# Kernel optimization log

Hardware: AMD Instinct MI355X
Metric: run time of the kernel (lower is better)

## Reference

```python
import jax, jax.numpy as jnp
import numpy as np
from jax import lax

DISP = 4   # max displacement for correlation -> 81 channels
KSZ = 3    # deform/gate conv kernel size


def conv2d(x, w, b=None):
    out = lax.conv_general_dilated(x, w, (1, 1), 'SAME',
                                   dimension_numbers=('NCHW', 'OIHW', 'NCHW'))
    if b is not None:
        out = out + b[None, :, None, None]
    return out


def correlation(x1, x2, d=DISP):
    # FlowNet-style cost volume, kernel_size=1: per-displacement channel-mean dot product.
    B, C, H, W = x1.shape
    x2p = jnp.pad(x2, ((0, 0), (0, 0), (d, d), (d, d)))
    outs = []
    for dy in range(2 * d + 1):
        for dx in range(2 * d + 1):
            shifted = lax.dynamic_slice(x2p, (0, 0, dy, dx), (B, C, H, W))
            outs.append(jnp.sum(x1 * shifted, axis=1) / C)
    return jnp.stack(outs, axis=1)  # [B, (2d+1)^2, H, W]


def bilinear_sample(img, y, x):
    # img: [B,C,H,W]; y,x: [B,H,W] float sample coords; zero padding outside.
    B, C, H, W = img.shape
    y0 = jnp.floor(y); x0 = jnp.floor(x)
    y1 = y0 + 1.0;     x1 = x0 + 1.0
    wy1 = y - y0; wx1 = x - x0
    wy0 = 1.0 - wy1; wx0 = 1.0 - wx1
    flat = img.reshape(B, C, H * W)

    def gather(yi, xi):
        valid = (yi >= 0) & (yi <= H - 1) & (xi >= 0) & (xi <= W - 1)
        yc = jnp.clip(yi, 0, H - 1).astype(jnp.int32)
        xc = jnp.clip(xi, 0, W - 1).astype(jnp.int32)
        idx = (yc * W + xc).reshape(B, 1, H * W)
        g = jnp.take_along_axis(flat, idx, axis=2).reshape(B, C, H, W)
        return g * valid.astype(img.dtype)[:, None]

    return (gather(y0, x0) * (wy0 * wx0)[:, None]
          + gather(y0, x1) * (wy0 * wx1)[:, None]
          + gather(y1, x0) * (wy1 * wx0)[:, None]
          + gather(y1, x1) * (wy1 * wx1)[:, None])


def deform_conv(img, offset, w, k=KSZ):
    # offset: [B, 2*k*k, H, W] with (dy, dx) pairs per kernel tap (row-major).
    B, C, H, W = img.shape
    pad = (k - 1) // 2
    ys = jnp.arange(H, dtype=img.dtype)[None, :, None]
    xs = jnp.arange(W, dtype=img.dtype)[None, None, :]
    out = jnp.zeros((B, w.shape[0], H, W), dtype=img.dtype)
    for kk in range(k * k):
        ky, kx = kk // k, kk % k
        y = ys + (ky - pad) + offset[:, 2 * kk]
        x = xs + (kx - pad) + offset[:, 2 * kk + 1]
        s = bilinear_sample(img, y, x)
        out = out + jnp.einsum('oc,bchw->bohw', w[:, :, ky, kx], s)
    return out


def linear_scale(x, std_multiplier=3.0):
    pos = x > 0
    cnt = jnp.sum(pos).astype(x.dtype)
    mean = jnp.sum(jnp.where(pos, x, 0.0)) / jnp.maximum(cnt, 1.0)
    var = jnp.sum(jnp.where(pos, (x - mean) ** 2, 0.0)) / jnp.maximum(cnt - 1.0, 1.0)
    ub = mean + std_multiplier * jnp.sqrt(var)
    ub = jnp.where(cnt >= 2.0, ub, 1.0)  # matches torch nan / empty-positive fallback
    return jnp.clip(x, 0.0, lax.stop_gradient(ub)) / ub


def setup_inputs() -> dict:
    key = jax.random.key(0)
    ks = jax.random.split(key, 10)
    B, C, H, W = 8, 256, 64, 64
    f = jnp.float32
    inp = {
        'inputs':   jax.random.normal(ks[0], (B, C, H, W), f),
        'in_state': jax.random.normal(ks[1], (B, C, H, W), f),
        'w_reset':  jax.random.normal(ks[2], (C, 2 * C, 3, 3), f) * 0.02,
        'b_reset':  jnp.zeros((C,), f),
        'w_update': jax.random.normal(ks[3], (C, 2 * C, 3, 3), f) * 0.02,
        'b_update': jnp.zeros((C,), f),
        'w_out':    jax.random.normal(ks[4], (C, 2 * C, 3, 3), f) * 0.02,
        'b_out':    jnp.zeros((C,), f),
        'w_offset': jax.random.normal(ks[5], (18, 81, 1, 1), f) * 0.01,
        'w_align':  jax.random.normal(ks[6], (C, C, 3, 3), f) * 0.01,
    }
    return inp


def reference(inputs, in_state, w_reset, b_reset, w_update, b_update,
              w_out, b_out, w_offset, w_align):
    # align_features: correlation -> 1x1 offset conv -> deformable conv
    corr = correlation(inputs, in_state)
    offset = conv2d(corr, w_offset)
    aligned = deform_conv(in_state, offset, w_align)
    # ConvGRU gates with linear-scaled relu gates
    stacked = jnp.concatenate([inputs, aligned], axis=1)
    update = linear_scale(jax.nn.relu(conv2d(stacked, w_update, b_update)))
    reset = linear_scale(jax.nn.relu(conv2d(stacked, w_reset, b_reset)))
    out_in = jax.nn.relu(conv2d(jnp.concatenate([inputs, in_state * reset], axis=1), w_out, b_out))
    new_state = in_state * (1.0 - update) + out_in * update
    return (new_state, new_state)  # (out_feat, new_state)
```

## Files before the change

kernel.cpp:

```cpp
#include <hip/hip_runtime.h>
#include <stdint.h>
#include <math.h>

typedef unsigned short u16;
typedef short bf16x8 __attribute__((ext_vector_type(8)));
typedef float f32x4 __attribute__((ext_vector_type(4)));

#define MFMA16x16x32(a,b,c) __builtin_amdgcn_mfma_f32_16x16x32_bf16((a),(b),(c),0,0,0)

typedef __attribute__((address_space(3))) void as3_void;
typedef const __attribute__((address_space(1))) void as1_void;

__device__ __forceinline__ void g2l16(const void* g, void* l){
#if __has_builtin(__builtin_amdgcn_global_load_lds)
  __builtin_amdgcn_global_load_lds((as1_void*)g, (as3_void*)l, 16, 0, 0);
#else
  *(int4*)l = *(const int4*)g;
#endif
}

__device__ __forceinline__ u16 f2bf(float f){
  uint32_t u = __builtin_bit_cast(uint32_t, f);
  u += 0x7fffu + ((u >> 16) & 1u);
  return (u16)(u >> 16);
}
__device__ __forceinline__ float bf2f(u16 h){
  uint32_t u = ((uint32_t)h) << 16;
  return __builtin_bit_cast(float, u);
}
__device__ __forceinline__ void unpack8(int4 v, float* o){
  uint32_t w0=(uint32_t)v.x, w1=(uint32_t)v.y, w2=(uint32_t)v.z, w3=(uint32_t)v.w;
  o[0]=__builtin_bit_cast(float, w0<<16); o[1]=__builtin_bit_cast(float, w0&0xffff0000u);
  o[2]=__builtin_bit_cast(float, w1<<16); o[3]=__builtin_bit_cast(float, w1&0xffff0000u);
  o[4]=__builtin_bit_cast(float, w2<<16); o[5]=__builtin_bit_cast(float, w2&0xffff0000u);
  o[6]=__builtin_bit_cast(float, w3<<16); o[7]=__builtin_bit_cast(float, w3&0xffff0000u);
}
__device__ __forceinline__ int iclampi(int v,int lo,int hi){ return v<lo?lo:(v>hi?hi:v); }

__global__ void k_repack(const float* __restrict__ w_reset, const float* __restrict__ b_reset,
                         const float* __restrict__ w_update, const float* __restrict__ b_update,
                         const float* __restrict__ w_out, const float* __restrict__ w_offset,
                         const float* __restrict__ w_align,
                         u16* __restrict__ wgate, u16* __restrict__ wout,
                         u16* __restrict__ walign, float* __restrict__ woff,
                         float* __restrict__ biascat){
  int idx = blockIdx.x * 256 + threadIdx.x;
  if (idx < 512*4608){
    int e = idx & 7, j = (idx >> 3) & 2047, chunk = idx >> 14;
    int nb = chunk & 1, kk = chunk >> 1;
    int l = j & 15, q = (j >> 4) & 3, t16 = (j >> 6) & 15, ks2 = j >> 10;
    int n = nb*256 + t16*16 + l;
    int tap = kk >> 3, ksin = kk & 7;
    int c = ksin*64 + ks2*32 + q*8 + e;
    int ky = tap/3, kx = tap%3;
    float v = (n < 256) ? w_update[((n*512 + c)*3 + ky)*3 + kx]
                        : w_reset[(((n-256)*512 + c)*3 + ky)*3 + kx];
    wgate[idx] = f2bf(v);
  }
  if (idx < 256*4608){
    int e = idx & 7, j = (idx >> 3) & 1023, chunk = idx >> 13;
    int nb = chunk & 1, kk = chunk >> 1;
    int l = j & 15, q = (j >> 4) & 3, t8 = (j >> 6) & 7, ks2 = j >> 9;
    int n = nb*128 + t8*16 + l;
    int tap = kk >> 3, ksin = kk & 7;
    int c = ksin*64 + ks2*32 + q*8 + e;
    int ky = tap/3, kx = tap%3;
    wout[idx] = f2bf(w_out[((n*512 + c)*3 + ky)*3 + kx]);
  }
  if (idx < 256*2304){
    int n = idx / 2304, k = idx % 2304;
    int tap = k >> 8, c = k & 255;
    int ky = tap/3, kx = tap%3;
    walign[idx] = f2bf(w_align[((n*256 + c)*3 + ky)*3 + kx]);
  }
  if (idx < 1458) woff[idx] = w_offset[idx] * (1.f/256.f);
  if (idx < 512) biascat[idx] = (idx < 256) ? b_update[idx] : b_reset[idx-256];
}

__global__ __launch_bounds__(256) void k_transform(const float* __restrict__ inputs,
    const float* __restrict__ in_state, u16* __restrict__ stacked,
    u16* __restrict__ stacked2, u16* __restrict__ x2pad){
  __shared__ u16 t1[64*264];
  __shared__ u16 t2[64*264];
  int tid = threadIdx.x, bh = blockIdx.x;
  int b = bh >> 6, h = bh & 63;
  int w = tid & 63, cq = tid >> 6;
  for (int i = 0; i < 64; ++i){
    int c = i*4 + cq;
    int gi = ((b*256 + c)*64 + h)*64 + w;
    t1[w*264 + c] = f2bf(inputs[gi]);
    t2[w*264 + c] = f2bf(in_state[gi]);
  }
  __syncthreads();
  int px = tid >> 2, cg = tid & 3;
#pragma unroll
  for (int u = 0; u < 8; ++u){
    int c = cg*64 + u*8;
    int4 v1 = *(const int4*)(t1 + px*264 + c);
    int4 v2 = *(const int4*)(t2 + px*264 + c);
    *(int4*)(stacked  + (((b*66 + h+1)*66) + (px+1))*512 + c) = v1;
    *(int4*)(stacked2 + (((b*66 + h+1)*66) + (px+1))*512 + c) = v1;
    *(int4*)(x2pad    + (((b*72 + h+4)*72) + (px+4))*256 + c) = v2;
  }
}

__global__ __launch_bounds__(256) void k_corr(const u16* __restrict__ stacked,
    const u16* __restrict__ x2pad, float* __restrict__ corr){
  __shared__ u16 lA[8192];
  __shared__ u16 lB[32768];
  int tid = threadIdx.x, idx = blockIdx.x;
  int b = idx >> 6, ty = (idx >> 3) & 7, tx = idx & 7;
  int h0 = ty*8, w0 = tx*8;
  int wave = tid >> 6, lane = tid & 63, l15 = lane & 15, quad = lane >> 4;
  f32x4 acc[4][4];
#pragma unroll
  for (int i=0;i<4;i++)
#pragma unroll
    for (int j=0;j<4;j++){ f32x4 z = {0.f,0.f,0.f,0.f}; acc[i][j] = z; }

  for (int s = 0; s < 2; ++s){
#pragma unroll
    for (int i = 0; i < 4; ++i){
      int j = tid + i*256;
      int ml = j & 15, q = (j>>4)&3, mt = (j>>6)&3, ks = j >> 8;
      int px = mt*16 + ml, py = px >> 3, pxx = px & 7;
      const u16* g = stacked + (((b*66 + h0+py+1)*66) + (w0+pxx+1))*512 + s*128 + ks*32 + q*8;
      g2l16(g, lA + j*8);
    }
#pragma unroll
    for (int i = 0; i < 16; ++i){
      int j = tid + i*256;
      int nl = j & 15, q = (j>>4)&3, nt = (j>>6)&15, ks = j >> 10;
      int qp = nt*16 + nl, qy = qp >> 4, qx = qp & 15;
      const u16* g = x2pad + (((b*72 + h0+qy)*72) + (w0+qx))*256 + s*128 + ks*32 + q*8;
      g2l16(g, lB + j*8);
    }
    __syncthreads();
#pragma unroll
    for (int ks = 0; ks < 4; ++ks){
      bf16x8 bv[4];
#pragma unroll
      for (int ni=0; ni<4; ++ni){
        int nt = wave*4 + ni;
        bv[ni] = *(const bf16x8*)(lB + (((ks*16 + nt)*4 + quad)*16 + l15)*8);
      }
#pragma unroll
      for (int mi=0; mi<4; ++mi){
        bf16x8 av = *(const bf16x8*)(lA + (((ks*4 + mi)*4 + quad)*16 + l15)*8);
#pragma unroll
        for (int ni=0; ni<4; ++ni) acc[mi][ni] = MFMA16x16x32(av, bv[ni], acc[mi][ni]);
      }
    }
    __syncthreads();
  }
#pragma unroll
  for (int mi=0; mi<4; ++mi){
#pragma unroll
    for (int ni=0; ni<4; ++ni){
      int n = wave*64 + ni*16 + l15;
      int qy = n >> 4, qx = n & 15;
#pragma unroll
      for (int r=0; r<4; ++r){
        int m = mi*16 + quad*4 + r;
        int py = m >> 3, pxx = m & 7;
        int dy = qy - py, dx = qx - pxx;
        if ((unsigned)dy <= 8u && (unsigned)dx <= 8u)
          corr[(((b*64 + h0+py)*64) + (w0+pxx))*81 + dy*9 + dx] = acc[mi][ni][r];
      }
    }
  }
}

__global__ __launch_bounds__(256) void k_offset(const float* __restrict__ corr,
    const float* __restrict__ woff, float* __restrict__ offs){
  __shared__ float lc[32*84];
  __shared__ float lw[18*84];
  int tid = threadIdx.x, blk = blockIdx.x;
  int row = blk >> 1, half = blk & 1;
  int base = row*5184 + half*32*81;
  for (int i = tid; i < 32*81; i += 256){
    int px = i / 81, d = i % 81;
    lc[px*84 + d] = corr[base + i];
  }
  for (int i = tid; i < 18*84; i += 256){
    int o = i / 84, d = i % 84;
    if (d < 81) lw[i] = woff[o*81 + d];
  }
  __syncthreads();
  int px = tid & 31, og = tid >> 5;
  for (int o = og; o < 18; o += 8){
    float s = 0.f;
#pragma unroll
    for (int dd = 0; dd < 20; ++dd){
      float4 a = *(const float4*)(lc + px*84 + dd*4);
      float4 wv = *(const float4*)(lw + o*84 + dd*4);
      s += a.x*wv.x + a.y*wv.y + a.z*wv.z + a.w*wv.w;
    }
    s += lc[px*84 + 80] * lw[o*84 + 80];
    offs[(row*64 + half*32 + px)*18 + o] = s;
  }
}

__global__ __launch_bounds__(256) void k_deform(const u16* __restrict__ x2pad,
    const float* __restrict__ offs, const u16* __restrict__ walign,
    u16* __restrict__ stacked){
  __shared__ u16 lA[16384];
  int tid = threadIdx.x, bh = blockIdx.x;
  int b = bh >> 6, h = bh & 63;
  int wave = tid >> 6, lane = tid & 63, l15 = lane & 15, quad = lane >> 4;
  int px = tid >> 2, cg = tid & 3;
  int mt_s = px >> 4, ml_s = px & 15;
  f32x4 acc[4][4];
#pragma unroll
  for (int i=0;i<4;i++)
#pragma unroll
    for (int j=0;j<4;j++){ f32x4 z = {0.f,0.f,0.f,0.f}; acc[i][j] = z; }

  for (int tap = 0; tap < 9; ++tap){
    int ky = tap/3, kx = tap%3;
    float offy = offs[(bh*64 + px)*18 + 2*tap];
    float offx = offs[(bh*64 + px)*18 + 2*tap + 1];
    float y = (float)(h + ky - 1) + offy;
    float x = (float)(px + kx - 1) + offx;
    float y0f = floorf(y), x0f = floorf(x);
    float wy1 = y - y0f, wx1 = x - x0f;
    float wy0 = 1.f - wy1, wx0 = 1.f - wx1;
    int iy0 = iclampi((int)y0f, -4, 67), ix0 = iclampi((int)x0f, -4, 67);
    int iy1 = iclampi((int)y0f + 1, -4, 67), ix1 = iclampi((int)x0f + 1, -4, 67);
    const u16* p00 = x2pad + (((b*72 + iy0+4)*72) + (ix0+4))*256 + cg*64;
    const u16* p01 = x2pad + (((b*72 + iy0+4)*72) + (ix1+4))*256 + cg*64;
    const u16* p10 = x2pad + (((b*72 + iy1+4)*72) + (ix0+4))*256 + cg*64;
    const u16* p11 = x2pad + (((b*72 + iy1+4)*72) + (ix1+4))*256 + cg*64;
    float w00 = wy0*wx0, w01 = wy0*wx1, w10 = wy1*wx0, w11 = wy1*wx1;
#pragma unroll
    for (int u = 0; u < 8; ++u){
      int4 v00 = *(const int4*)(p00 + u*8);
      int4 v01 = *(const int4*)(p01 + u*8);
      int4 v10 = *(const int4*)(p10 + u*8);
      int4 v11 = *(const int4*)(p11 + u*8);
      float a00[8], a01[8], a10[8], a11[8];
      unpack8(v00,a00); unpack8(v01,a01); unpack8(v10,a10); unpack8(v11,a11);
      union { u16 h2[8]; int4 v; } R;
#pragma unroll
      for (int jj = 0; jj < 8; ++jj)
        R.h2[jj] = f2bf(w00*a00[jj] + w01*a01[jj] + w10*a10[jj] + w11*a11[jj]);
      int ch = cg*64 + u*8;
      int ks = ch >> 5, q = (ch >> 3) & 3;
      *(int4*)(lA + (((ks*4 + mt_s)*4 + q)*16 + ml_s)*8) = R.v;
    }
    __syncthreads();
#pragma unroll
    for (int ks = 0; ks < 8; ++ks){
      bf16x8 bv[4];
#pragma unroll
      for (int ni=0; ni<4; ++ni){
        int n = wave*64 + ni*16 + l15;
        bv[ni] = *(const bf16x8*)(walign + n*2304 + tap*256 + ks*32 + quad*8);
      }
#pragma unroll
      for (int mi=0; mi<4; ++mi){
        bf16x8 av = *(const bf16x8*)(lA + (((ks*4 + mi)*4 + quad)*16 + l15)*8);
#pragma unroll
        for (int ni=0; ni<4; ++ni) acc[mi][ni] = MFMA16x16x32(av, bv[ni], acc[mi][ni]);
      }
    }
    __syncthreads();
  }
#pragma unroll
  for (int mi=0; mi<4; ++mi){
#pragma unroll
    for (int ni=0; ni<4; ++ni){
      int n = wave*64 + ni*16 + l15;
#pragma unroll
      for (int r=0; r<4; ++r){
        int m = mi*16 + quad*4 + r;
        stacked[(((b*66 + h+1)*66) + (m+1))*512 + 256 + n] = f2bf(acc[mi][ni][r]);
      }
    }
  }
}

__device__ __forceinline__ void stageA_cl(u16* __restrict__ dst,
    const u16* __restrict__ in, int b, int h0, int kk, int tid){
  int tap = kk >> 3, ksin = kk & 7;
  int ky = tap/3, kx = tap - ky*3;
  const u16* abase = in + ((b*66 + h0 + ky)*66 + kx)*512 + ksin*64;
#pragma unroll
  for (int i = 0; i < 4; ++i){
    int j = i*512 + tid;
    int px = j >> 3, i8 = j & 7;
    int c8 = i8 ^ (px & 7);
    int r = px >> 6, w = px & 63;
    g2l16(abase + (r*66 + w)*512 + c8*8, dst + j*8);
  }
}
__device__ __forceinline__ void stageB16_k(u16* __restrict__ dst,
    const u16* __restrict__ wts, int nb, int kk, int ks2, int tid){
  const u16* wch = wts + (size_t)(kk*2 + nb) * 16384;
#pragma unroll
  for (int i = 0; i < 2; ++i){
    int j = (ks2<<10) | (i<<9) | tid;
    g2l16(wch + j*8, dst + j*8);
  }
}
__device__ __forceinline__ void stageB8_k(u16* __restrict__ dst,
    const u16* __restrict__ wts, int nb, int kk, int ks2, int tid){
  const u16* wch = wts + (size_t)(kk*2 + nb) * 8192;
  int j = (ks2<<9) | tid;
  g2l16(wch + j*8, dst + j*8);
}

#define AVREAD(RA, MROW, K2) \
  (*(const bf16x8*)((const u16*)(RA) + (MROW)*1024 + l15*64 + \
    ((((K2)*32) + quad*8) ^ ((l15 & 7)*8))))

#define PH16(CMH, AVC, BVC, AVN, BVN, LOADB, RA, RB, NMH, NK2, STG, EPI) do { \
  _Pragma("unroll") \
  for (int m4_=0;m4_<4;++m4_) \
    AVN[m4_] = AVREAD(RA, wm*8 + (NMH)*4 + m4_, NK2); \
  if (LOADB){ \
    _Pragma("unroll") \
    for (int ni_=0;ni_<4;++ni_) \
      BVN[ni_] = *(const bf16x8*)((const u16*)(RB) + ((((NK2)*16 + wn*4 + ni_)*4 + quad)*16 + l15)*8); \
  } \
  STG; \
  __builtin_amdgcn_sched_barrier(0); \
  __builtin_amdgcn_s_setprio(1); \
  _Pragma("unroll") \
  for (int m4_=0;m4_<4;++m4_){ \
    _Pragma("unroll") \
    for (int ni_=0;ni_<4;++ni_) \
      acc[(CMH)*4+m4_][ni_] = MFMA16x16x32(AVC[m4_], BVC[ni_], acc[(CMH)*4+m4_][ni_]); \
  } \
  __builtin_amdgcn_s_setprio(0); \
  __builtin_amdgcn_sched_barrier(0); \
  EPI; \
} while(0)

#define PH8Q(CMH, AVC, BVC, AVN, BVN, LOADB, RA, RB, NMH, NK2, STG, EPI) do { \
  _Pragma("unroll") \
  for (int m4_=0;m4_<4;++m4_) \
    AVN[m4_] = AVREAD(RA, wm*8 + (NMH)*4 + m4_, NK2); \
  if (LOADB){ \
    _Pragma("unroll") \
    for (int ni_=0;ni_<2;++ni_) \
      BVN[ni_] = *(const bf16x8*)((const u16*)(RB) + ((((NK2)*8 + wn*2 + ni_)*4 + quad)*16 + l15)*8); \
  } \
  STG; \
  __builtin_amdgcn_sched_barrier(0); \
  __builtin_amdgcn_s_setprio(1); \
  _Pragma("unroll") \
  for (int m4_=0;m4_<4;++m4_){ \
    _Pragma("unroll") \
    for (int ni_=0;ni_<2;++ni_) \
      acc[(CMH)*4+m4_][ni_] = MFMA16x16x32(AVC[m4_], BVC[ni_], acc[(CMH)*4+m4_][ni_]); \
  } \
  __builtin_amdgcn_s_setprio(0); \
  __builtin_amdgcn_sched_barrier(0); \
  EPI; \
} while(0)

#define SYNCTILE do { \
  __syncthreads(); \
  __builtin_amdgcn_sched_barrier(0); \
} while(0)

template<int NT, bool STATS>
__global__ __launch_bounds__(512, 2) void k_conv256(const u16* __restrict__ in,
    const u16* __restrict__ wts, const float* __restrict__ bias,
    u16* __restrict__ outp, float* __restrict__ partials){
  constexpr int NI = NT / 4;
  __shared__ u16 lA[2][16384];
  __shared__ u16 lB[2][NT*1024];

  int tid = threadIdx.x, g = blockIdx.x;
  int work = (g & 7) * 32 + (g >> 3);
  int nb = work >> 7, mt = work & 127;
  int b = mt >> 4, h0 = (mt & 15) * 4;
  int wave = tid >> 6, lane = tid & 63, l15 = lane & 15, quad = lane >> 4;
  int wm = wave & 1, wn = wave >> 1;

  f32x4 acc[8][NI];
#pragma unroll
  for (int i=0;i<8;i++)
#pragma unroll
    for (int j=0;j<NI;j++){ f32x4 z = {0.f,0.f,0.f,0.f}; acc[i][j] = z; }

  if constexpr (NT == 16){
    bf16x8 avA[4], avB[4], bvA[4], bvB[4];
    stageA_cl(&lA[0][0], in, b, h0, 0, tid);
    stageB16_k(&lB[0][0], wts, nb, 0, 0, tid);
    stageB16_k(&lB[0][0], wts, nb, 0, 1, tid);
    __syncthreads();
#pragma unroll
    for (int m4_=0;m4_<4;++m4_)
      avA[m4_] = AVREAD(&lA[0][0], wm*8 + m4_, 0);
#pragma unroll
    for (int ni_=0;ni_<4;++ni_)
      bvA[ni_] = *(const bf16x8*)(&lB[0][0] + (((wn*4 + ni_)*4 + quad)*16 + l15)*8);

#pragma unroll 1
    for (int t = 0; t < 72; ++t){
      int d = t & 1;
      const u16* Acur = &lA[d][0];
      const u16* Bcur = &lB[d][0];
      u16* Anx = &lA[d^1][0];
      u16* Bnx = &lB[d^1][0];
      bool hn = (t < 71);
      int kn = t + 1;
      PH16(0, avA, bvA, avB, bvB, 0, Acur, Bcur, 1, 0,
           if (hn){ stageA_cl(Anx, in, b, h0, kn, tid);
                    stageB16_k(Bnx, wts, nb, kn, 0, tid);
                    stageB16_k(Bnx, wts, nb, kn, 1, tid); }, );
      PH16(1, avB, bvA, avA, bvB, 1, Acur, Bcur, 0, 1, , );
      PH16(0, avA, bvB, avB, bvA, 0, Acur, Bcur, 1, 1, , SYNCTILE);
      PH16(1, avB, bvB, avA, bvA, 1, Anx, Bnx, 0, 0, , );
    }
  } else {
    bf16x8 avA[4], avB[4], bvA[2], bvB[2];
    stageA_cl(&lA[0][0], in, b, h0, 0, tid);
    stageB8_k(&lB[0][0], wts, nb, 0, 0, tid);
    stageB8_k(&lB[0][0], wts, nb, 0, 1, tid);
    __syncthreads();
#pragma unroll
    for (int m4_=0;m4_<4;++m4_)
      avA[m4_] = AVREAD(&lA[0][0], wm*8 + m4_, 0);
#pragma unroll
    for (int ni_=0;ni_<2;++ni_)
      bvA[ni_] = *(const bf16x8*)(&lB[0][0] + (((wn*2 + ni_)*4 + quad)*16 + l15)*8);

#pragma unroll 1
    for (int t = 0; t < 72; ++t){
      int d = t & 1;
      const u16* Acur = &lA[d][0];
      const u16* Bcur = &lB[d][0];
      u16* Anx = &lA[d^1][0];
      u16* Bnx = &lB[d^1][0];
      bool hn = (t < 71);
      int kn = t + 1;
      PH8Q(0, avA, bvA, avB, bvB, 0, Acur, Bcur, 1, 0,
           if (hn){ stageA_cl(Anx, in, b, h0, kn, tid);
                    stageB8_k(Bnx, wts, nb, kn, 0, tid);
                    stageB8_k(Bnx, wts, nb, kn, 1, tid); }, );
      PH8Q(1, avB, bvA, avA, bvB, 1, Acur, Bcur, 0, 1, , );
      PH8Q(0, avA, bvB, avB, bvA, 0, Acur, Bcur, 1, 1, , SYNCTILE);
      PH8Q(1, avB, bvB, avA, bvA, 1, Anx, Bnx, 0, 0, , );
    }
  }

  float bvl[NI];
#pragma unroll
  for (int ni = 0; ni < NI; ++ni)
    bvl[ni] = bias[nb*(NT*16) + wn*(NI*16) + ni*16 + l15];
  float sc = 0.f, ss = 0.f, sq = 0.f;
#pragma unroll
  for (int mi=0; mi<8; ++mi){
#pragma unroll
    for (int ni=0; ni<NI; ++ni){
      int n = nb*(NT*16) + wn*(NI*16) + ni*16 + l15;
#pragma unroll
      for (int r=0; r<4; ++r){
        int m = wm*128 + mi*16 + quad*4 + r;
        int row = h0 + (m >> 6), w = m & 63;
        float v = acc[mi][ni][r] + bvl[ni];
        v = fmaxf(v, 0.f);
        outp[(((b*64 + row)*64) + w)*(NT*32) + n] = f2bf(v);
        if (STATS){ sc += (v > 0.f) ? 1.f : 0.f; ss += v; sq += v*v; }
      }
    }
  }
  if constexpr (STATS){
    __shared__ float red[8][3];
#pragma unroll
    for (int off = 32; off; off >>= 1){
      sc += __shfl_down(sc, off); ss += __shfl_down(ss, off); sq += __shfl_down(sq, off);
    }
    if (lane == 0){ red[wave][0]=sc; red[wave][1]=ss; red[wave][2]=sq; }
    __syncthreads();
    if (tid == 0){
      float a0=0,a1=0,a2=0;
      for (int w2=0; w2<8; ++w2){ a0+=red[w2][0]; a1+=red[w2][1]; a2+=red[w2][2]; }
      partials[work*3+0]=a0; partials[work*3+1]=a1; partials[work*3+2]=a2;
    }
  }
}

__global__ __launch_bounds__(256) void k_finalize(const float* __restrict__ partials,
                                                  float* __restrict__ ubs){
  __shared__ float red[4][6];
  int tid = threadIdx.x, lane = tid & 63, wave = tid >> 6;
  float cu=0,su=0,qu=0,cr=0,sr=0,qr=0;
  {
    float c = partials[tid*3+0], s = partials[tid*3+1], q = partials[tid*3+2];
    if (tid < 128){ cu=c; su=s; qu=q; } else { cr=c; sr=s; qr=q; }
  }
#pragma unroll
  for (int off = 32; off; off >>= 1){
    cu += __shfl_down(cu, off); su += __shfl_down(su, off); qu += __shfl_down(qu, off);
    cr += __shfl_down(cr, off); sr += __shfl_down(sr, off); qr += __shfl_down(qr, off);
  }
  if (lane == 0){ red[wave][0]=cu; red[wave][1]=su; red[wave][2]=qu;
                  red[wave][3]=cr; red[wave][4]=sr; red[wave][5]=qr; }
  __syncthreads();
  if (tid < 2){
    double C=0, S=0, Q=0;
    for (int w2=0; w2<4; ++w2){
      C += red[w2][tid*3+0]; S += red[w2][tid*3+1]; Q += red[w2][tid*3+2];
    }
    float ub = 1.f;
    if (C >= 2.0){
      double mean = S / C;
      double var = (Q - C*mean*mean) / (C - 1.0);
      if (var < 0.0) var = 0.0;
      ub = (float)(mean + 3.0*sqrt(var));
    }
    ubs[tid] = ub;
    ubs[2+tid] = 1.f/ub;
  }
}

__global__ __launch_bounds__(256) void k_mulreset(const u16* __restrict__ G,
    const u16* __restrict__ x2pad, const float* __restrict__ ubs,
    u16* __restrict__ stacked2){
  int tid = threadIdx.x, bh = blockIdx.x;
  int b = bh >> 6, h = bh & 63;
  int px = tid >> 2, cg = tid & 3;
  float ubr = ubs[1], inv = ubs[3];
#pragma unroll
  for (int u = 0; u < 8; ++u){
    int c = cg*64 + u*8;
    int4 gv = *(const int4*)(G + (bh*64 + px)*512 + 256 + c);
    int4 sv = *(const int4*)(x2pad + (((b*72 + h+4)*72) + (px+4))*256 + c);
    float gf[8], sf[8]; unpack8(gv, gf); unpack8(sv, sf);
    union { u16 h2[8]; int4 v; } R;
#pragma unroll
    for (int j=0;j<8;j++){
      float r = fminf(gf[j], ubr) * inv;
      R.h2[j] = f2bf(sf[j] * r);
    }
    *(int4*)(stacked2 + (((b*66 + h+1)*66) + (px+1))*512 + 256 + c) = R.v;
  }
}

__global__ __launch_bounds__(256) void k_final(const u16* __restrict__ G,
    const u16* __restrict__ O, const float* __restrict__ in_state,
    const float* __restrict__ ubs, float* __restrict__ dout){
  __shared__ float Q[64*65];
  __shared__ float P[64*65];
  int tid = threadIdx.x, bh = blockIdx.x;
  int b = bh >> 6, h = bh & 63;
  float ubu = ubs[0], inv = ubs[2];
  int px = tid >> 2, cs = (tid & 3)*16;
  int w = tid & 63, c4 = tid >> 6;
  for (int cb = 0; cb < 4; ++cb){
#pragma unroll
    for (int tt = 0; tt < 2; ++tt){
      int cl = cs + tt*8;
      int c = cb*64 + cl;
      int4 gv = *(const int4*)(G + (bh*64 + px)*512 + c);
      int4 ov = *(const int4*)(O + (bh*64 + px)*256 + c);
      float gf[8], of[8]; unpack8(gv, gf); unpack8(ov, of);
#pragma unroll
      for (int j=0;j<8;j++){
        float u = fminf(gf[j], ubu) * inv;
        Q[px*65 + cl + j] = u;
        P[px*65 + cl + j] = of[j]*u;
      }
    }
    __syncthreads();
    for (int i = 0; i < 16; ++i){
      int cl = i*4 + c4;
      int c = cb*64 + cl;
      int gidx = (((b*256 + c)*64) + h)*64 + w;
      float s = in_state[gidx];
      float v = s*(1.f - Q[w*65 + cl]) + P[w*65 + cl];
      dout[gidx] = v;
      dout[8388608 + gidx] = v;
    }
    __syncthreads();
  }
}

extern "C" void kernel_launch(void* const* d_in, const int* in_sizes, int n_in,
                              void* d_out, int out_size, void* d_ws, size_t ws_size,
                              hipStream_t stream){
  (void)in_sizes; (void)n_in; (void)out_size; (void)ws_size;
  const float* inputs   = (const float*)d_in[0];
  const float* in_state = (const float*)d_in[1];
  const float* w_reset  = (const float*)d_in[2];
  const float* b_reset  = (const float*)d_in[3];
  const float* w_update = (const float*)d_in[4];
  const float* b_update = (const float*)d_in[5];
  const float* w_out    = (const float*)d_in[6];
  const float* b_out    = (const float*)d_in[7];
  const float* w_offset = (const float*)d_in[8];
  const float* w_align  = (const float*)d_in[9];
  float* dout = (float*)d_out;

  char* ws = (char*)d_ws;
  size_t off = 0;
  auto alloc = [&](size_t bytes)->char*{
    char* p = ws + off; off = (off + bytes + 255) & ~(size_t)255; return p;
  };
  const size_t x2pad_b   = 8ull*72*72*256*2;
  const size_t stacked_b = 8ull*66*66*512*2;
  u16* x2pad    = (u16*)alloc(x2pad_b);
  u16* stacked  = (u16*)alloc(stacked_b);
  u16* stacked2 = (u16*)alloc(stacked_b);
  float* corr   = (float*)alloc(8ull*64*64*81*4);
  float* offs   = (float*)alloc(8ull*64*64*18*4);
  u16* G        = (u16*)alloc(8ull*64*64*512*2);
  u16* O        = (u16*)alloc(8ull*64*64*256*2);
  u16* wgate    = (u16*)alloc(512ull*4608*2);
  u16* woutb    = (u16*)alloc(256ull*4608*2);
  u16* walignb  = (u16*)alloc(256ull*2304*2);
  float* woff   = (float*)alloc(1458*4);
  float* biascat= (float*)alloc(512*4);
  float* partials=(float*)alloc(1024*3*4);
  float* ubs    = (float*)alloc(4*4);

  hipMemsetAsync(x2pad,    0, x2pad_b,   stream);
  hipMemsetAsync(stacked,  0, stacked_b, stream);
  hipMemsetAsync(stacked2, 0, stacked_b, stream);

  k_repack<<<9216, 256, 0, stream>>>(w_reset, b_reset, w_update, b_update, w_out,
                                     w_offset, w_align, wgate, woutb, walignb, woff, biascat);
  k_transform<<<512, 256, 0, stream>>>(inputs, in_state, stacked, stacked2, x2pad);
  k_corr<<<512, 256, 0, stream>>>(stacked, x2pad, corr);
  k_offset<<<1024, 256, 0, stream>>>(corr, woff, offs);
  k_deform<<<512, 256, 0, stream>>>(x2pad, offs, walignb, stacked);
  k_conv256<16, true><<<256, 512, 0, stream>>>(stacked, wgate, biascat, G, partials);
  k_finalize<<<1, 256, 0, stream>>>(partials, ubs);
  k_mulreset<<<512, 256, 0, stream>>>(G, x2pad, ubs, stacked2);
  k_conv256<8, false><<<256, 512, 0, stream>>>(stacked2, woutb, b_out, O, nullptr);
  k_final<<<512, 256, 0, stream>>>(G, O, in_state, ubs, dout);
}
```

Baseline: 631.9 us.

## Double-buffer deform-conv LDS staging and swizzle layout with coalesced gathers

Restructures k_deform so that the bilinear gather for the next tap is staged into a second LDS buffer while MFMAs run on the current tap. Each barrier pair per tap becomes a single barrier. Gather lanes now read 8 contiguous channels per pixel across 32 lanes, giving coalesced 512-byte rows, and LDS writes use an XOR swizzle to avoid bank conflicts. The align weights are also pre-permuted so that B-fragment loads are contiguous per (tap, ks). The cost is double the LDS use, which may reduce occupancy.

Measured after the change: 568.8 us. -10.0%, faster.

```diff
diff --git a/kernel.cpp b/kernel.cpp
--- a/kernel.cpp
+++ b/kernel.cpp
@@ -68,8 +68,10 @@
     wout[idx] = f2bf(w_out[((n*512 + c)*3 + ky)*3 + kx]);
   }
   if (idx < 256*2304){
-    int n = idx / 2304, k = idx % 2304;
-    int tap = k >> 8, c = k & 255;
+    int u = idx >> 13, rem = idx & 8191;
+    int n = rem >> 5, qd = (rem >> 3) & 3, e = idx & 7;
+    int tap = u >> 3, ks = u & 7;
+    int c = ks*32 + qd*8 + e;
     int ky = tap/3, kx = tap%3;
     walign[idx] = f2bf(w_align[((n*256 + c)*3 + ky)*3 + kx]);
   }
@@ -204,66 +206,76 @@
 __global__ __launch_bounds__(256) void k_deform(const u16* __restrict__ x2pad,
     const float* __restrict__ offs, const u16* __restrict__ walign,
     u16* __restrict__ stacked){
-  __shared__ u16 lA[16384];
+  __shared__ u16 lA[2][16384];
   int tid = threadIdx.x, bh = blockIdx.x;
   int b = bh >> 6, h = bh & 63;
   int wave = tid >> 6, lane = tid & 63, l15 = lane & 15, quad = lane >> 4;
-  int px = tid >> 2, cg = tid & 3;
-  int mt_s = px >> 4, ml_s = px & 15;
+  int g8 = tid >> 5, c32 = tid & 31;
+  int ksw = c32 >> 2, qw = c32 & 3, x7 = c32 & 7;
   f32x4 acc[4][4];
 #pragma unroll
   for (int i=0;i<4;i++)
 #pragma unroll
     for (int j=0;j<4;j++){ f32x4 z = {0.f,0.f,0.f,0.f}; acc[i][j] = z; }
 
-  for (int tap = 0; tap < 9; ++tap){
-    int ky = tap/3, kx = tap%3;
-    float offy = offs[(bh*64 + px)*18 + 2*tap];
-    float offx = offs[(bh*64 + px)*18 + 2*tap + 1];
-    float y = (float)(h + ky - 1) + offy;
-    float x = (float)(px + kx - 1) + offx;
-    float y0f = floorf(y), x0f = floorf(x);
-    float wy1 = y - y0f, wx1 = x - x0f;
-    float wy0 = 1.f - wy1, wx0 = 1.f - wx1;
-    int iy0 = iclampi((int)y0f, -4, 67), ix0 = iclampi((int)x0f, -4, 67);
-    int iy1 = iclampi((int)y0f + 1, -4, 67), ix1 = iclampi((int)x0f + 1, -4, 67);
-    const u16* p00 = x2pad + (((b*72 + iy0+4)*72) + (ix0+4))*256 + cg*64;
-    const u16* p01 = x2pad + (((b*72 + iy0+4)*72) + (ix1+4))*256 + cg*64;
-    const u16* p10 = x2pad + (((b*72 + iy1+4)*72) + (ix0+4))*256 + cg*64;
-    const u16* p11 = x2pad + (((b*72 + iy1+4)*72) + (ix1+4))*256 + cg*64;
-    float w00 = wy0*wx0, w01 = wy0*wx1, w10 = wy1*wx0, w11 = wy1*wx1;
-#pragma unroll
-    for (int u = 0; u < 8; ++u){
-      int4 v00 = *(const int4*)(p00 + u*8);
-      int4 v01 = *(const int4*)(p01 + u*8);
-      int4 v10 = *(const int4*)(p10 + u*8);
-      int4 v11 = *(const int4*)(p11 + u*8);
+  auto STAGE = [&](u16* __restrict__ dst, int tap){
+    int ky = tap/3, kx = tap - ky*3;
+#pragma unroll 2
+    for (int pi = 0; pi < 8; ++pi){
+      int px = pi*8 + g8;
+      float offy = offs[(bh*64 + px)*18 + 2*tap];
+      float offx = offs[(bh*64 + px)*18 + 2*tap + 1];
+      float y = (float)(h + ky - 1) + offy;
+      float x = (float)(px + kx - 1) + offx;
+      float y0f = floorf(y), x0f = floorf(x);
+      float wy1 = y - y0f, wx1 = x - x0f;
+      float wy0 = 1.f - wy1, wx0 = 1.f - wx1;
+      int iy0 = iclampi((int)y0f, -4, 67), ix0 = iclampi((int)x0f, -4, 67);
+      int iy1 = iclampi((int)y0f + 1, -4, 67), ix1 = iclampi((int)x0f + 1, -4, 67);
+      const u16* p00 = x2pad + (((b*72 + iy0+4)*72) + (ix0+4))*256 + c32*8;
+      const u16* p01 = x2pad + (((b*72 + iy0+4)*72) + (ix1+4))*256 + c32*8;
+      const u16* p10 = x2pad + (((b*72 + iy1+4)*72) + (ix0+4))*256 + c32*8;
+      const u16* p11 = x2pad + (((b*72 + iy1+4)*72) + (ix1+4))*256 + c32*8;
+      int4 v00 = *(const int4*)p00;
+      int4 v01 = *(const int4*)p01;
+      int4 v10 = *(const int4*)p10;
+      int4 v11 = *(const int4*)p11;
+      float w00 = wy0*wx0, w01 = wy0*wx1, w10 = wy1*wx0, w11 = wy1*wx1;
       float a00[8], a01[8], a10[8], a11[8];
       unpack8(v00,a00); unpack8(v01,a01); unpack8(v10,a10); unpack8(v11,a11);
       union { u16 h2[8]; int4 v; } R;
 #pragma unroll
       for (int jj = 0; jj < 8; ++jj)
         R.h2[jj] = f2bf(w00*a00[jj] + w01*a01[jj] + w10*a10[jj] + w11*a11[jj]);
-      int ch = cg*64 + u*8;
-      int ks = ch >> 5, q = (ch >> 3) & 3;
-      *(int4*)(lA + (((ks*4 + mt_s)*4 + q)*16 + ml_s)*8) = R.v;
-    }
-    __syncthreads();
+      int mt = px >> 4, ml = px & 15;
+      *(int4*)(dst + ksw*2048 + mt*512 + qw*128 + (ml ^ x7)*8) = R.v;
+    }
+  };
+
+  STAGE(&lA[0][0], 0);
+  __syncthreads();
+
+  for (int tap = 0; tap < 9; ++tap){
+    int d = tap & 1;
+    if (tap < 8) STAGE(&lA[d^1][0], tap + 1);
+    const u16* A = &lA[d][0];
+    __builtin_amdgcn_s_setprio(1);
 #pragma unroll
     for (int ks = 0; ks < 8; ++ks){
       bf16x8 bv[4];
 #pragma unroll
       for (int ni=0; ni<4; ++ni){
         int n = wave*64 + ni*16 + l15;
-        bv[ni] = *(const bf16x8*)(walign + n*2304 + tap*256 + ks*32 + quad*8);
+        bv[ni] = *(const bf16x8*)(walign + (size_t)(tap*8 + ks)*8192 + n*32 + quad*8);
       }
 #pragma unroll
       for (int mi=0; mi<4; ++mi){
-        bf16x8 av = *(const bf16x8*)(lA + (((ks*4 + mi)*4 + quad)*16 + l15)*8);
+        bf16x8 av = *(const bf16x8*)(A + ks*2048 + mi*512 + quad*128 + (l15 ^ ((ks*4 + quad) & 7))*8);
 #pragma unroll
         for (int ni=0; ni<4; ++ni) acc[mi][ni] = MFMA16x16x32(av, bv[ni], acc[mi][ni]);
       }
     }
+    __builtin_amdgcn_s_setprio(0);
     __syncthreads();
   }
 #pragma unroll
```
